# Performance work log

Measured on AMD Instinct MI355X. Metric: run time of the kernel, lower is better.

## Reference

```python
import jax, jax.numpy as jnp
import numpy as np

B, N, E, H, F, L, S = 4, 384, 768, 32, 3072, 12, 512
D = E // H


def setup_inputs() -> dict:
    key = jax.random.key(0)
    ks = jax.random.split(key, 32)
    inp = {}
    # forward args
    inp['node_type'] = jax.random.randint(ks[0], (B, N, 1), 1, S + 1)  # table has S+1 rows; 0 = pad (unused)
    inp['node_input_feature'] = jax.random.normal(ks[1], (B, N, E), jnp.float32)
    inp['in_degree'] = jax.random.randint(ks[2], (B, N), 0, S)
    inp['out_degree'] = jax.random.randint(ks[3], (B, N), 0, S)
    inp['attn_bias'] = jax.random.normal(ks[4], (B, N, N), jnp.float32) * 0.1
    inp['spatial_pos'] = jax.random.randint(ks[5], (B, N, N), 0, S)
    # embedding tables (normal stddev 0.02, as in the flax module)
    inp['node_emb'] = jax.random.normal(ks[6], (S + 1, E), jnp.float32) * 0.02
    inp['in_deg_emb'] = jax.random.normal(ks[7], (S, E), jnp.float32) * 0.02
    inp['out_deg_emb'] = jax.random.normal(ks[8], (S, E), jnp.float32) * 0.02
    inp['sp_emb'] = jax.random.normal(ks[9], (S, H), jnp.float32) * 0.02
    inp['sp_emb_rev'] = jax.random.normal(ks[10], (S, H), jnp.float32) * 0.02
    # per-layer weights, stacked along leading L axis
    se, sf = 1.0 / np.sqrt(E), 1.0 / np.sqrt(F)
    inp['Wq'] = jax.random.normal(ks[11], (L, E, E), jnp.float32) * se
    inp['bq'] = jax.random.normal(ks[12], (L, E), jnp.float32) * se
    inp['Wk'] = jax.random.normal(ks[13], (L, E, E), jnp.float32) * se
    inp['bk'] = jax.random.normal(ks[14], (L, E), jnp.float32) * se
    inp['Wv'] = jax.random.normal(ks[15], (L, E, E), jnp.float32) * se
    inp['bv'] = jax.random.normal(ks[16], (L, E), jnp.float32) * se
    inp['Wo'] = jax.random.normal(ks[17], (L, E, E), jnp.float32) * se
    inp['bo'] = jnp.zeros((L, E), jnp.float32)
    inp['W1'] = jax.random.normal(ks[18], (L, E, F), jnp.float32) * se
    inp['b1'] = jax.random.normal(ks[19], (L, F), jnp.float32) * se
    inp['W2'] = jax.random.normal(ks[20], (L, F, E), jnp.float32) * sf
    inp['b2'] = jax.random.normal(ks[21], (L, E), jnp.float32) * sf
    inp['ln1_s'] = jnp.ones((L, E), jnp.float32)
    inp['ln1_b'] = jnp.zeros((L, E), jnp.float32)
    inp['ln2_s'] = jnp.ones((L, E), jnp.float32)
    inp['ln2_b'] = jnp.zeros((L, E), jnp.float32)
    return inp


def _layernorm(x, scale, bias, eps=1e-5):
    m = x.mean(-1, keepdims=True)
    v = ((x - m) ** 2).mean(-1, keepdims=True)
    return (x - m) / jnp.sqrt(v + eps) * scale + bias


def _encoder(node_type, node_input_feature, in_degree, out_degree, attn_bias, spatial_pos,
             node_emb, in_deg_emb, out_deg_emb, sp_emb, sp_emb_rev,
             Wq, bq, Wk, bk, Wv, bv, Wo, bo, W1, b1, W2, b2, ln1_s, ln1_b, ln2_s, ln2_b):
    nt = node_type[..., 0]                               # [B,N]
    padding_mask = nt == 0                               # [B,N]
    # node features: node_emb(node_type).sum(-2) + degree embeddings + input feature
    x = (node_emb[node_type].sum(axis=-2)
         + in_deg_emb[in_degree] + out_deg_emb[out_degree]
         + node_input_feature)                           # [B,N,E]
    # spatial attention bias: [B,N,N,H] -> [B,H,N,N], plus graph-level attn_bias
    sb = sp_emb[spatial_pos] + sp_emb_rev[jnp.transpose(spatial_pos, (0, 2, 1))]
    bias = jnp.transpose(sb, (0, 3, 1, 2)) + attn_bias[:, None]  # [B,H,N,N]

    x = jnp.transpose(x, (1, 0, 2))                      # [N,B,E]
    scaling = D ** (-0.5)
    neg_inf = jnp.float32(-jnp.inf)

    def layer(x, p):
        wq, bq_, wk, bk_, wv, bv_, wo, bo_, w1, b1_, w2, b2_, s1, t1, s2, t2 = p
        q = ((x @ wq) + bq_) * scaling                   # [N,B,E], bias scaled too (faithful)
        k = (x @ wk) + bk_
        v = (x @ wv) + bv_
        q = q.reshape(N, B, H, D)
        k = k.reshape(N, B, H, D)
        v = v.reshape(N, B, H, D)
        w = jnp.einsum('nbhd,mbhd->bhnm', q, k) + bias   # [B,H,N,N]
        w = jnp.where(padding_mask[:, None, None, :], neg_inf, w)
        probs = jax.nn.softmax(w.astype(jnp.float32), axis=-1).astype(x.dtype)
        a = jnp.einsum('bhnm,mbhd->nbhd', probs, v).reshape(N, B, E)
        a = a @ wo + bo_
        x = _layernorm(x + a, s1, t1)                    # post-LN
        h = jax.nn.gelu(x @ w1 + b1_)                    # approximate gelu (flax default)
        h = h @ w2 + b2_
        x = _layernorm(x + h, s2, t2)
        return x, None

    xs = (Wq, bq, Wk, bk, Wv, bv, Wo, bo, W1, b1, W2, b2, ln1_s, ln1_b, ln2_s, ln2_b)
    x, _ = jax.lax.scan(layer, x, xs)
    return x                                             # [N,B,E]


def reference(node_type, node_input_feature, in_degree, out_degree, attn_bias, spatial_pos,
              node_emb, in_deg_emb, out_deg_emb, sp_emb, sp_emb_rev,
              Wq, bq, Wk, bk, Wv, bv, Wo, bo, W1, b1, W2, b2, ln1_s, ln1_b, ln2_s, ln2_b):
    return _encoder(node_type, node_input_feature, in_degree, out_degree, attn_bias, spatial_pos,
                    node_emb, in_deg_emb, out_deg_emb, sp_emb, sp_emb_rev,
                    Wq, bq, Wk, bk, Wv, bv, Wo, bo, W1, b1, W2, b2, ln1_s, ln1_b, ln2_s, ln2_b)
```

## Files before the change

kernel.cpp:

```cpp
#include <hip/hip_runtime.h>
#include <hip/hip_bf16.h>

#define Bb 4
#define Nn 384
#define Ee 768
#define Hh 32
#define Ff 3072
#define Ll 12
#define Ss 512
#define Mm (Nn*Bb)

typedef __attribute__((ext_vector_type(8))) short bf16x8;
typedef __attribute__((ext_vector_type(4))) float f32x4;
typedef unsigned short u16;

__device__ __forceinline__ u16 f2b(float f) {
  union { float f; unsigned int i; } c; c.f = f;
  unsigned int x = c.i;
  return (u16)((x + 0x7fffu + ((x >> 16) & 1u)) >> 16);
}
__device__ __forceinline__ float b2f(u16 u) {
  union { unsigned int i; float f; } c; c.i = ((unsigned int)u) << 16; return c.f;
}
__device__ __forceinline__ unsigned pkcvt(float lo, float hi) {
  unsigned r;
  asm("v_cvt_pk_bf16_f32 %0, %1, %2" : "=v"(r) : "v"(lo), "v"(hi));
  return r;
}
__device__ __forceinline__ void gload_lds16(const void* g, void* l) {
  __builtin_amdgcn_global_load_lds((__attribute__((address_space(1))) void*)(g),
                                   (__attribute__((address_space(3))) void*)(l), 16, 0, 0);
}

__global__ __launch_bounds__(256) void embed_kernel(
    const int* __restrict__ node_type, const float* __restrict__ nif,
    const int* __restrict__ in_deg, const int* __restrict__ out_deg,
    const float* __restrict__ node_emb, const float* __restrict__ ind_emb,
    const float* __restrict__ outd_emb,
    float* __restrict__ x, u16* __restrict__ xb)
{
  const int r = blockIdx.x;
  const int n = r / Bb, b = r % Bb;
  const int nt  = node_type[b*Nn + n];
  const int idg = in_deg[b*Nn + n];
  const int odg = out_deg[b*Nn + n];
  for (int c = threadIdx.x; c < Ee; c += 256) {
    float val = node_emb[(size_t)nt*Ee + c] + ind_emb[(size_t)idg*Ee + c]
              + outd_emb[(size_t)odg*Ee + c] + nif[((size_t)b*Nn + n)*Ee + c];
    x[(size_t)r*Ee + c] = val;
    xb[(size_t)r*Ee + c] = f2b(val);
  }
}

__global__ void spT_kernel(const int* __restrict__ sp, int* __restrict__ spT)
{
  __shared__ int tile[32][33];
  const int b = blockIdx.z;
  const int n0 = blockIdx.y * 32, m0 = blockIdx.x * 32;
  const int tx = threadIdx.x, ty = threadIdx.y;
  for (int i = ty; i < 32; i += 8)
    tile[i][tx] = sp[((size_t)b*Nn + n0 + i)*Nn + m0 + tx];
  __syncthreads();
  for (int i = ty; i < 32; i += 8)
    spT[((size_t)b*Nn + m0 + i)*Nn + n0 + tx] = tile[tx][i];
}

__global__ __launch_bounds__(256) void bias_pre_kernel(
    const float* __restrict__ atb, const int* __restrict__ sp, const int* __restrict__ spT,
    const float* __restrict__ sp_emb, const float* __restrict__ sp_emb_rev,
    u16* __restrict__ biasb)
{
  __shared__ float spc[512], sprc[512];
  const int bx = blockIdx.x, h = blockIdx.y, b = blockIdx.z;
  const int t = threadIdx.x;
  for (int i = t; i < 512; i += 256) {
    spc[i]  = sp_emb[(size_t)i*Hh + h];
    sprc[i] = sp_emb_rev[(size_t)i*Hh + h];
  }
  __syncthreads();
  const int q = bx*16 + ((t >> 2) & 15);
  const size_t rowb = ((size_t)b*Nn + q)*Nn;
  u16* outb = biasb + (((size_t)(b*Hh + h)*24 + bx)*24)*256 + t;
  const int mbase = ((t >> 6) << 2) + (t & 3);
  for (int tt = 0; tt < 24; ++tt) {
    const int m = tt*16 + mbase;
    float v = atb[rowb + m] + spc[sp[rowb + m]] + sprc[spT[rowb + m]];
    outb[tt*256] = f2b(v);
  }
}

__global__ __launch_bounds__(256) void wconv_kernel(
    const float* __restrict__ Wq, const float* __restrict__ Wk, const float* __restrict__ Wv,
    const float* __restrict__ Wo, const float* __restrict__ W1, const float* __restrict__ W2,
    int layer0, u16* __restrict__ wTall, unsigned slotStride)
{
  __shared__ float tile[64][65];
  const int layer = layer0 + blockIdx.y;
  u16* slot = wTall + (size_t)blockIdx.y * slotStride;
  int tid = blockIdx.x;
  const float* src; u16* dst; int Ns, Ks;
  if (tid < 432)       { int seg = tid / 144; tid -= seg*144;
                         src = (seg==0?Wq:(seg==1?Wk:Wv)) + (size_t)layer*Ee*Ee;
                         dst = slot + (size_t)seg*589824; Ns = 768; Ks = 768; }
  else if (tid < 576)  { tid -= 432; src = Wo + (size_t)layer*Ee*Ee; dst = slot + 1769472; Ns = 768;  Ks = 768; }
  else if (tid < 1152) { tid -= 576; src = W1 + (size_t)layer*Ee*Ff; dst = slot + 2359296; Ns = 3072; Ks = 768; }
  else                 { tid -= 1152; src = W2 + (size_t)layer*Ff*Ee; dst = slot + 4718592; Ns = 768; Ks = 3072; }
  const int tc = Ns >> 6;
  const int tk = tid / tc, tn = tid % tc;
  const int t = threadIdx.x;
  #pragma unroll
  for (int i = 0; i < 4; ++i) {
    const int id = t + i*256;
    const int r = id >> 4, c = (id & 15) << 2;
    float4 v = *(const float4*)(src + (size_t)(tk*64 + r)*Ns + tn*64 + c);
    tile[r][c+0] = v.x; tile[r][c+1] = v.y; tile[r][c+2] = v.z; tile[r][c+3] = v.w;
  }
  __syncthreads();
  #pragma unroll
  for (int i = 0; i < 2; ++i) {
    const int ch = t + i*256;
    const int n = ch >> 3, kc = (ch & 7) << 3;
    uint4 u;
    u.x = pkcvt(tile[kc+0][n], tile[kc+1][n]);
    u.y = pkcvt(tile[kc+2][n], tile[kc+3][n]);
    u.z = pkcvt(tile[kc+4][n], tile[kc+5][n]);
    u.w = pkcvt(tile[kc+6][n], tile[kc+7][n]);
    *(uint4*)(dst + (size_t)(tn*64 + n)*Ks + tk*64 + kc) = u;
  }
}

template<int EPI>
__global__ __launch_bounds__(256) void gemm3_kernel(
    const u16* __restrict__ A, const u16* __restrict__ Bw,
    const float* __restrict__ b0, const float* __restrict__ b1, const float* __restrict__ b2,
    int Kfull, int Kc, float scaleQ,
    float* __restrict__ outF, u16* __restrict__ outB)
{
  __shared__ __align__(16) u16 As[2][128][64];
  __shared__ __align__(16) u16 Bs[2][64][64];
  const int t = threadIdx.x, lane = t & 63, wave = t >> 6;
  int bx = blockIdx.x, by = blockIdx.y;
  {
    const int gx = gridDim.x;
    const int nwg = gx * gridDim.y;
    const int bid = bx + gx * by;
    const int cpx = nwg >> 3;
    const int s = (bid & 7) * cpx + (bid >> 3);
    bx = s % gx; by = s / gx;
  }
  const int m0 = bx * 128, n0 = by * 64;
  const int k0 = blockIdx.z * Kc;
  const int wm = wave >> 1, wn = wave & 1;
  const int ql = lane & 15, hi = lane >> 4;
  const int nk = Kc >> 6;
  const int sr = t >> 3;
  const int sslot = (t & 7) ^ (sr & 7);
  const size_t aoff = (size_t)(m0 + sr)*Kfull + k0 + (sslot << 3);
  const size_t boff = (size_t)(n0 + sr)*Kfull + k0 + (sslot << 3);
  const size_t rstep = (size_t)32 * Kfull;

  int aro[4][2], bro[2][2];
  #pragma unroll
  for (int ks = 0; ks < 2; ++ks) {
    const int kb = (((ks<<2) + hi) ^ (ql & 7)) << 4;
    #pragma unroll
    for (int f = 0; f < 4; ++f) aro[f][ks] = (wm*64 + f*16 + ql)*128 + kb;
    #pragma unroll
    for (int f = 0; f < 2; ++f) bro[f][ks] = (wn*32 + f*16 + ql)*128 + kb;
  }

  f32x4 acc[4][2];
  #pragma unroll
  for (int a = 0; a < 4; ++a)
    #pragma unroll
    for (int c = 0; c < 2; ++c) acc[a][c] = (f32x4){0.f,0.f,0.f,0.f};

  #pragma unroll
  for (int i = 0; i < 4; ++i)
    gload_lds16(A + aoff + i*rstep, (char*)&As[0][0][0] + i*4096 + t*16);
  #pragma unroll
  for (int i = 0; i < 2; ++i)
    gload_lds16(Bw + boff + i*rstep, (char*)&Bs[0][0][0] + i*4096 + t*16);

  for (int kt = 0; kt < nk; ++kt) {
    const int cur = kt & 1, nxt = cur ^ 1;
    const bool pre = (kt + 1 < nk);
    if (pre) {
      const size_t kk = (size_t)(kt + 1) << 6;
      #pragma unroll
      for (int i = 0; i < 4; ++i)
        gload_lds16(A + aoff + kk + i*rstep, (char*)&As[nxt][0][0] + i*4096 + t*16);
      #pragma unroll
      for (int i = 0; i < 2; ++i)
        gload_lds16(Bw + boff + kk + i*rstep, (char*)&Bs[nxt][0][0] + i*4096 + t*16);
      asm volatile("s_waitcnt vmcnt(6)" ::: "memory");
    } else {
      asm volatile("s_waitcnt vmcnt(0)" ::: "memory");
    }
    __builtin_amdgcn_s_barrier();
    __builtin_amdgcn_sched_barrier(0);

    const char* aBase = (const char*)&As[cur][0][0];
    const char* bBase = (const char*)&Bs[cur][0][0];
    bf16x8 af[4][2], bf[2][2];
    #pragma unroll
    for (int f = 0; f < 4; ++f)
      #pragma unroll
      for (int ks = 0; ks < 2; ++ks)
        af[f][ks] = *(const bf16x8*)(aBase + aro[f][ks]);
    #pragma unroll
    for (int f = 0; f < 2; ++f)
      #pragma unroll
      for (int ks = 0; ks < 2; ++ks)
        bf[f][ks] = *(const bf16x8*)(bBase + bro[f][ks]);
    #pragma unroll
    for (int ks = 0; ks < 2; ++ks)
      #pragma unroll
      for (int fm = 0; fm < 4; ++fm)
        #pragma unroll
        for (int fn = 0; fn < 2; ++fn)
          acc[fm][fn] = __builtin_amdgcn_mfma_f32_16x16x32_bf16(af[fm][ks], bf[fn][ks], acc[fm][fn], 0, 0, 0);
    if (pre) {
      __builtin_amdgcn_sched_barrier(0);
      __builtin_amdgcn_s_barrier();
    }
  }

  #pragma unroll
  for (int fm = 0; fm < 4; ++fm) {
    const int rowb = m0 + wm*64 + fm*16 + hi*4;
    #pragma unroll
    for (int fn = 0; fn < 2; ++fn) {
      const int gcol = n0 + wn*32 + fn*16 + ql;
      float bv, scale = 1.0f;
      if (EPI == 0) {
        const int seg = gcol / 768;
        const int cw = gcol - seg*768;
        bv = (seg == 0) ? b0[cw] : ((seg == 1) ? b1[cw] : b2[cw]);
        if (seg == 0) scale = scaleQ;
      } else if (EPI == 1) {
        bv = (blockIdx.z == 0) ? b0[gcol] : 0.0f;
      } else {
        bv = b0[gcol];
      }
      f32x4 v = acc[fm][fn];
      #pragma unroll
      for (int j = 0; j < 4; ++j) {
        float val = (v[j] + bv) * scale;
        if (EPI == 0) {
          outB[(size_t)(rowb + j) * 2304 + gcol] = f2b(val);
        } else if (EPI == 1) {
          outF[(size_t)blockIdx.z * (Mm*768) + (size_t)(rowb + j) * 768 + gcol] = val;
        } else {
          float arg = 0.7978845608028654f * (val + 0.044715f * val * val * val);
          float e = __expf(2.0f * arg);
          float g = 0.5f * val * (2.0f - 2.0f / (e + 1.0f));
          outB[(size_t)(rowb + j) * 3072 + gcol] = f2b(g);
        }
      }
    }
  }
}

template<int PREBIAS>
__global__ __launch_bounds__(256) void attn2_kernel(
    const u16* __restrict__ qkv,
    const u16* __restrict__ biasb,
    const float* __restrict__ atb, const int* __restrict__ sp, const int* __restrict__ spT,
    const float* __restrict__ sp_emb, const float* __restrict__ sp_emb_rev,
    u16* __restrict__ ab)
{
  __shared__ __align__(16) u16 Kt[384][32];
  __shared__ __align__(16) u16 Vt[32][392];
  __shared__ __align__(16) u16 Qt[64][32];
  __shared__ __align__(16) u16 Pw[4][16][32];
  __shared__ float spc[512], sprc[512];
  const int bid = blockIdx.x;
  const int pair = bid % 3;
  const int h = (bid / 3) % Hh;
  const int b = bid / (3 * Hh);
  const int t = threadIdx.x, lane = t & 63, wave = t >> 6;
  const int ql = lane & 15, hi = lane >> 4;

  for (int idx = t; idx < 384*6; idx += 256) {
    const int m = idx / 6, c = idx - m*6;
    const u16* base = qkv + ((size_t)m*Bb + b)*2304 + h*24 + c*4;
    uint2 kk = *(const uint2*)(base + 768);
    uint2 vv = *(const uint2*)(base + 1536);
    *(uint2*)&Kt[m][c*4] = kk;
    Vt[c*4+0][m] = (u16)(vv.x & 0xffffu); Vt[c*4+1][m] = (u16)(vv.x >> 16);
    Vt[c*4+2][m] = (u16)(vv.y & 0xffffu); Vt[c*4+3][m] = (u16)(vv.y >> 16);
  }
  for (int idx = t; idx < 384*2; idx += 256)
    *(uint2*)&Kt[idx>>1][24 + (idx&1)*4] = make_uint2(0u, 0u);
  for (int idx = t; idx < 8*196; idx += 256)
    *(unsigned*)((char*)&Vt[24][0] + idx*4) = 0u;
  if (!PREBIAS) {
    for (int i = t; i < 512; i += 256) {
      spc[i]  = sp_emb[(size_t)i*Hh + h];
      sprc[i] = sp_emb_rev[(size_t)i*Hh + h];
    }
  }

  for (int qi = 0; qi < 2; ++qi) {
    const int ntile = pair*2 + qi;
    for (int idx = t; idx < 64*6; idx += 256) {
      const int qr = idx / 6, c = idx - qr*6;
      const u16* base = qkv + ((size_t)(ntile*64 + qr)*Bb + b)*2304 + h*24 + c*4;
      *(uint2*)&Qt[qr][c*4] = *(const uint2*)base;
    }
    for (int idx = t; idx < 64*2; idx += 256)
      *(uint2*)&Qt[idx>>1][24 + (idx&1)*4] = make_uint2(0u, 0u);
    __syncthreads();

    const int q0 = ntile*64 + wave*16;
    const int q = q0 + ql;
    const bf16x8 qf = *(const bf16x8*)&Qt[wave*16 + ql][hi*8];

    f32x4 f[24];
    const u16* bp = biasb + (((size_t)(b*Hh + h)*24 + ntile*4 + wave)*24)*256 + lane*4;
    const size_t crow = ((size_t)b*Nn + q)*Nn;
    #pragma unroll
    for (int tt = 0; tt < 24; ++tt) {
      bf16x8 kf = *(const bf16x8*)&Kt[tt*16 + ql][hi*8];
      f32x4 z = (f32x4){0.f,0.f,0.f,0.f};
      f32x4 s = __builtin_amdgcn_mfma_f32_16x16x32_bf16(kf, qf, z, 0, 0, 0);
      if (PREBIAS) {
        uint2 bb = *(const uint2*)(bp + tt*256);
        s[0] += b2f((u16)(bb.x & 0xffffu)); s[1] += b2f((u16)(bb.x >> 16));
        s[2] += b2f((u16)(bb.y & 0xffffu)); s[3] += b2f((u16)(bb.y >> 16));
      } else {
        const int off = tt*16 + hi*4;
        int4 s4 = *(const int4*)(sp + crow + off);
        int4 t4 = *(const int4*)(spT + crow + off);
        float4 a4 = *(const float4*)(atb + crow + off);
        s[0] += a4.x + spc[s4.x] + sprc[t4.x];
        s[1] += a4.y + spc[s4.y] + sprc[t4.y];
        s[2] += a4.z + spc[s4.z] + sprc[t4.z];
        s[3] += a4.w + spc[s4.w] + sprc[t4.w];
      }
      f[tt] = s;
    }

    float mx = -3.0e38f;
    #pragma unroll
    for (int tt = 0; tt < 24; ++tt)
      mx = fmaxf(mx, fmaxf(fmaxf(f[tt][0], f[tt][1]), fmaxf(f[tt][2], f[tt][3])));
    mx = fmaxf(mx, __shfl_xor(mx, 16, 64));
    mx = fmaxf(mx, __shfl_xor(mx, 32, 64));
    float sum = 0.f;
    #pragma unroll
    for (int tt = 0; tt < 24; ++tt) {
      #pragma unroll
      for (int j = 0; j < 4; ++j) { f[tt][j] = __expf(f[tt][j] - mx); sum += f[tt][j]; }
    }
    sum += __shfl_xor(sum, 16, 64);
    sum += __shfl_xor(sum, 32, 64);
    const float inv = 1.0f / sum;

    f32x4 o0 = (f32x4){0.f,0.f,0.f,0.f}, o1 = (f32x4){0.f,0.f,0.f,0.f};
    char* prow = (char*)&Pw[wave][ql][0];
    const int swz = (ql & 3) << 4;
    #pragma unroll
    for (int c = 0; c < 12; ++c) {
      unsigned w0 = pkcvt(f[2*c][0],   f[2*c][1]);
      unsigned w1 = pkcvt(f[2*c][2],   f[2*c][3]);
      unsigned w2 = pkcvt(f[2*c+1][0], f[2*c+1][1]);
      unsigned w3 = pkcvt(f[2*c+1][2], f[2*c+1][3]);
      *(unsigned*)(prow + (((hi*8)      ) ^ swz)) = w0;
      *(unsigned*)(prow + (((hi*8) +  4) ^ swz)) = w1;
      *(unsigned*)(prow + (((hi*8) + 32) ^ swz)) = w2;
      *(unsigned*)(prow + (((hi*8) + 36) ^ swz)) = w3;
      bf16x8 a = *(const bf16x8*)(prow + ((hi*16) ^ swz));
      bf16x8 v0 = *(const bf16x8*)&Vt[ql][c*32 + hi*8];
      bf16x8 v1 = *(const bf16x8*)&Vt[16 + ql][c*32 + hi*8];
      o0 = __builtin_amdgcn_mfma_f32_16x16x32_bf16(a, v0, o0, 0, 0, 0);
      o1 = __builtin_amdgcn_mfma_f32_16x16x32_bf16(a, v1, o1, 0, 0, 0);
    }

    #pragma unroll
    for (int j = 0; j < 4; ++j) {
      float invj = __shfl(inv, hi*4 + j, 64);
      const int qg = q0 + hi*4 + j;
      u16* orow = ab + ((size_t)qg*Bb + b)*Ee + h*24;
      orow[ql] = f2b(o0[j] * invj);
      if (ql < 8) orow[16 + ql] = f2b(o1[j] * invj);
    }
    __syncthreads();
  }
}

template<int NP>
__global__ __launch_bounds__(256) void ln_kernel(
    const float* __restrict__ xin, const float* __restrict__ delta,
    const float* __restrict__ gamma, const float* __restrict__ beta,
    float* __restrict__ xout, u16* __restrict__ xb)
{
  __shared__ float red[8];
  const int r = blockIdx.x, t = threadIdx.x;
  const size_t base = (size_t)r * Ee;
  float v[3];
  #pragma unroll
  for (int i = 0; i < 3; ++i) {
    int c = t + i*256;
    float d = xin[base + c];
    #pragma unroll
    for (int p = 0; p < NP; ++p) d += delta[(size_t)p*(Mm*768) + base + c];
    v[i] = d;
  }
  float s = v[0] + v[1] + v[2];
  #pragma unroll
  for (int off = 1; off < 64; off <<= 1) s += __shfl_xor(s, off, 64);
  if ((t & 63) == 0) red[t >> 6] = s;
  __syncthreads();
  const float mean = (red[0] + red[1] + red[2] + red[3]) * (1.0f / 768.0f);
  float qs = 0.f;
  #pragma unroll
  for (int i = 0; i < 3; ++i) { float d = v[i] - mean; qs += d * d; }
  #pragma unroll
  for (int off = 1; off < 64; off <<= 1) qs += __shfl_xor(qs, off, 64);
  if ((t & 63) == 0) red[4 + (t >> 6)] = qs;
  __syncthreads();
  const float var = (red[4] + red[5] + red[6] + red[7]) * (1.0f / 768.0f);
  const float rstd = rsqrtf(var + 1e-5f);
  #pragma unroll
  for (int i = 0; i < 3; ++i) {
    int c = t + i*256;
    float o = (v[i] - mean) * rstd * gamma[c] + beta[c];
    xout[base + c] = o;
    xb[base + c] = f2b(o);
  }
}

extern "C" void kernel_launch(void* const* d_in, const int* in_sizes, int n_in,
                              void* d_out, int out_size, void* d_ws, size_t ws_size,
                              hipStream_t stream) {
  const int*   node_type  = (const int*)d_in[0];
  const float* nif        = (const float*)d_in[1];
  const int*   in_deg     = (const int*)d_in[2];
  const int*   out_deg    = (const int*)d_in[3];
  const float* atb        = (const float*)d_in[4];
  const int*   sp         = (const int*)d_in[5];
  const float* node_emb   = (const float*)d_in[6];
  const float* ind_emb    = (const float*)d_in[7];
  const float* outd_emb   = (const float*)d_in[8];
  const float* sp_emb     = (const float*)d_in[9];
  const float* sp_emb_rev = (const float*)d_in[10];
  const float* Wq = (const float*)d_in[11]; const float* bq = (const float*)d_in[12];
  const float* Wk = (const float*)d_in[13]; const float* bk = (const float*)d_in[14];
  const float* Wv = (const float*)d_in[15]; const float* bv = (const float*)d_in[16];
  const float* Wo = (const float*)d_in[17]; const float* bo = (const float*)d_in[18];
  const float* W1 = (const float*)d_in[19]; const float* b1 = (const float*)d_in[20];
  const float* W2 = (const float*)d_in[21]; const float* b2 = (const float*)d_in[22];
  const float* ln1s = (const float*)d_in[23]; const float* ln1b = (const float*)d_in[24];
  const float* ln2s = (const float*)d_in[25]; const float* ln2b = (const float*)d_in[26];

  char* ws = (char*)d_ws;
  float* x      = (float*)(ws);
  u16*   xb     = (u16*)(ws +  4718592);
  u16*   qkvb16 = (u16*)(ws +  7077888);
  u16*   abuf   = (u16*)(ws + 14155776);
  u16*   hb     = (u16*)(ws + 16515072);
  float* obufP  = (float*)(ws + 25952256);
  int*   spTb   = (int*)(ws + 44826624);
  u16*   biasb  = (u16*)(ws + 47185920);
  const bool useBias = ws_size >= 99090432ull;
  const bool allW    = ws_size >= 254803968ull;
  u16* wTall = (u16*)(ws + (useBias ? 84934656 : 47185920));
  const unsigned LSLOT = 7077888u;

  embed_kernel<<<Mm, 256, 0, stream>>>(node_type, nif, in_deg, out_deg,
                                       node_emb, ind_emb, outd_emb, x, xb);
  spT_kernel<<<dim3(12, 12, 4), dim3(32, 8), 0, stream>>>(sp, spTb);
  if (useBias)
    bias_pre_kernel<<<dim3(24, 32, 4), 256, 0, stream>>>(atb, sp, spTb, sp_emb, sp_emb_rev, biasb);
  if (allW)
    wconv_kernel<<<dim3(1728, 12), 256, 0, stream>>>(Wq, Wk, Wv, Wo, W1, W2,
                                                     0, wTall, LSLOT);

  const float scaleQ = 0.2041241452319315f;

  for (int l = 0; l < Ll; ++l) {
    const float *bql = bq + (size_t)l*Ee, *bkl = bk + (size_t)l*Ee, *bvl = bv + (size_t)l*Ee;
    const float *bol = bo + (size_t)l*Ee;
    const float *b1l = b1 + (size_t)l*Ff, *b2l = b2 + (size_t)l*Ee;

    if (!allW)
      wconv_kernel<<<dim3(1728, 1), 256, 0, stream>>>(Wq, Wk, Wv, Wo, W1, W2,
                                                      l, wTall, 0u);
    u16* slot = wTall + (size_t)(allW ? l : 0) * LSLOT;
    const u16* qkvT = slot;
    const u16* woT  = slot + 1769472;
    const u16* w1T  = slot + 2359296;
    const u16* w2T  = slot + 4718592;

    gemm3_kernel<0><<<dim3(12, 36), 256, 0, stream>>>(xb, qkvT, bql, bkl, bvl,
                                                      768, 768, scaleQ, nullptr, qkvb16);
    if (useBias)
      attn2_kernel<1><<<384, 256, 0, stream>>>(qkvb16, biasb, atb, sp, spTb,
                                               sp_emb, sp_emb_rev, abuf);
    else
      attn2_kernel<0><<<384, 256, 0, stream>>>(qkvb16, nullptr, atb, sp, spTb,
                                               sp_emb, sp_emb_rev, abuf);
    gemm3_kernel<1><<<dim3(12, 12, 2), 256, 0, stream>>>(abuf, woT, bol, bol, bol,
                                                         768, 384, 1.0f, obufP, nullptr);
    ln_kernel<2><<<Mm, 256, 0, stream>>>(x, obufP, ln1s + (size_t)l*Ee, ln1b + (size_t)l*Ee, x, xb);
    gemm3_kernel<2><<<dim3(12, 48), 256, 0, stream>>>(xb, w1T, b1l, b1l, b1l,
                                                      768, 768, 1.0f, nullptr, hb);
    gemm3_kernel<1><<<dim3(12, 12, 4), 256, 0, stream>>>(hb, w2T, b2l, b2l, b2l,
                                                         3072, 768, 1.0f, obufP, nullptr);
    float* xdst = (l == Ll - 1) ? (float*)d_out : x;
    ln_kernel<4><<<Mm, 256, 0, stream>>>(x, obufP, ln2s + (size_t)l*Ee, ln2b + (size_t)l*Ee, xdst, xb);
  }
}
```

Baseline: 1.347 ms.

## Widen GEMM tile to 128x128 with 512 threads, batch weight conversion tiles

```diff
diff --git a/kernel.cpp b/kernel.cpp
--- a/kernel.cpp
+++ b/kernel.cpp
@@ -89,6 +89,22 @@
   }
 }
 
+__device__ __forceinline__ void wc_resolve(int tid, int layer,
+    const float* Wq, const float* Wk, const float* Wv, const float* Wo,
+    const float* W1, const float* W2, u16* slot,
+    const float*& src, u16*& dst, int& Ns, int& Ks, int& tk, int& tn)
+{
+  if (tid < 432)      { int seg = tid/144; int r = tid - seg*144;
+                        src = (seg==0?Wq:(seg==1?Wk:Wv)) + (size_t)layer*Ee*Ee;
+                        dst = slot + (size_t)seg*589824; Ns=768; Ks=768; tk=r/12; tn=r%12; }
+  else if (tid < 576) { int r = tid-432;  src = Wo + (size_t)layer*Ee*Ee;
+                        dst = slot + 1769472; Ns=768;  Ks=768;  tk=r/12; tn=r%12; }
+  else if (tid < 1152){ int r = tid-576;  src = W1 + (size_t)layer*Ee*Ff;
+                        dst = slot + 2359296; Ns=3072; Ks=768;  tk=r/48; tn=r%48; }
+  else                { int r = tid-1152; src = W2 + (size_t)layer*Ff*Ee;
+                        dst = slot + 4718592; Ns=768;  Ks=3072; tk=r/12; tn=r%12; }
+}
+
 __global__ __launch_bounds__(256) void wconv_kernel(
     const float* __restrict__ Wq, const float* __restrict__ Wk, const float* __restrict__ Wv,
     const float* __restrict__ Wo, const float* __restrict__ W1, const float* __restrict__ W2,
@@ -97,47 +113,56 @@
   __shared__ float tile[64][65];
   const int layer = layer0 + blockIdx.y;
   u16* slot = wTall + (size_t)blockIdx.y * slotStride;
-  int tid = blockIdx.x;
-  const float* src; u16* dst; int Ns, Ks;
-  if (tid < 432)       { int seg = tid / 144; tid -= seg*144;
-                         src = (seg==0?Wq:(seg==1?Wk:Wv)) + (size_t)layer*Ee*Ee;
-                         dst = slot + (size_t)seg*589824; Ns = 768; Ks = 768; }
-  else if (tid < 576)  { tid -= 432; src = Wo + (size_t)layer*Ee*Ee; dst = slot + 1769472; Ns = 768;  Ks = 768; }
-  else if (tid < 1152) { tid -= 576; src = W1 + (size_t)layer*Ee*Ff; dst = slot + 2359296; Ns = 3072; Ks = 768; }
-  else                 { tid -= 1152; src = W2 + (size_t)layer*Ff*Ee; dst = slot + 4718592; Ns = 768; Ks = 3072; }
-  const int tc = Ns >> 6;
-  const int tk = tid / tc, tn = tid % tc;
   const int t = threadIdx.x;
-  #pragma unroll
-  for (int i = 0; i < 4; ++i) {
-    const int id = t + i*256;
-    const int r = id >> 4, c = (id & 15) << 2;
-    float4 v = *(const float4*)(src + (size_t)(tk*64 + r)*Ns + tn*64 + c);
-    tile[r][c+0] = v.x; tile[r][c+1] = v.y; tile[r][c+2] = v.z; tile[r][c+3] = v.w;
-  }
-  __syncthreads();
-  #pragma unroll
-  for (int i = 0; i < 2; ++i) {
-    const int ch = t + i*256;
-    const int n = ch >> 3, kc = (ch & 7) << 3;
-    uint4 u;
-    u.x = pkcvt(tile[kc+0][n], tile[kc+1][n]);
-    u.y = pkcvt(tile[kc+2][n], tile[kc+3][n]);
-    u.z = pkcvt(tile[kc+4][n], tile[kc+5][n]);
-    u.w = pkcvt(tile[kc+6][n], tile[kc+7][n]);
-    *(uint4*)(dst + (size_t)(tn*64 + n)*Ks + tk*64 + kc) = u;
+  const int lr = t >> 4, c0 = (t & 15) << 2;
+  const int tid0 = blockIdx.x * 6;
+
+  const float* src; u16* dst; int Ns, Ks, tk, tn;
+  wc_resolve(tid0, layer, Wq, Wk, Wv, Wo, W1, W2, slot, src, dst, Ns, Ks, tk, tn);
+  float4 rg[4];
+  #pragma unroll
+  for (int i = 0; i < 4; ++i)
+    rg[i] = *(const float4*)(src + (size_t)(tk*64 + lr + i*16)*Ns + tn*64 + c0);
+
+  for (int it = 0; it < 6; ++it) {
+    u16* dstC = dst; const int KsC = Ks, tkC = tk, tnC = tn;
+    __syncthreads();
+    #pragma unroll
+    for (int i = 0; i < 4; ++i) {
+      float4 v = rg[i];
+      const int r = lr + i*16;
+      tile[r][c0+0] = v.x; tile[r][c0+1] = v.y; tile[r][c0+2] = v.z; tile[r][c0+3] = v.w;
+    }
+    if (it + 1 < 6) {
+      wc_resolve(tid0 + it + 1, layer, Wq, Wk, Wv, Wo, W1, W2, slot, src, dst, Ns, Ks, tk, tn);
+      #pragma unroll
+      for (int i = 0; i < 4; ++i)
+        rg[i] = *(const float4*)(src + (size_t)(tk*64 + lr + i*16)*Ns + tn*64 + c0);
+    }
+    __syncthreads();
+    #pragma unroll
+    for (int i = 0; i < 2; ++i) {
+      const int ch = t + i*256;
+      const int n = ch >> 3, kc = (ch & 7) << 3;
+      uint4 u;
+      u.x = pkcvt(tile[kc+0][n], tile[kc+1][n]);
+      u.y = pkcvt(tile[kc+2][n], tile[kc+3][n]);
+      u.z = pkcvt(tile[kc+4][n], tile[kc+5][n]);
+      u.w = pkcvt(tile[kc+6][n], tile[kc+7][n]);
+      *(uint4*)(dstC + (size_t)(tnC*64 + n)*KsC + tkC*64 + kc) = u;
+    }
   }
 }
 
 template<int EPI>
-__global__ __launch_bounds__(256) void gemm3_kernel(
+__global__ __launch_bounds__(512) void gemm4_kernel(
     const u16* __restrict__ A, const u16* __restrict__ Bw,
     const float* __restrict__ b0, const float* __restrict__ b1, const float* __restrict__ b2,
     int Kfull, int Kc, float scaleQ,
     float* __restrict__ outF, u16* __restrict__ outB)
 {
   __shared__ __align__(16) u16 As[2][128][64];
-  __shared__ __align__(16) u16 Bs[2][64][64];
+  __shared__ __align__(16) u16 Bs[2][128][64];
   const int t = threadIdx.x, lane = t & 63, wave = t >> 6;
   int bx = blockIdx.x, by = blockIdx.y;
   {
@@ -148,16 +173,16 @@
     const int s = (bid & 7) * cpx + (bid >> 3);
     bx = s % gx; by = s / gx;
   }
-  const int m0 = bx * 128, n0 = by * 64;
+  const int m0 = bx * 128, n0 = by * 128;
   const int k0 = blockIdx.z * Kc;
-  const int wm = wave >> 1, wn = wave & 1;
+  const int wm = wave >> 2, wn = wave & 3;
   const int ql = lane & 15, hi = lane >> 4;
   const int nk = Kc >> 6;
   const int sr = t >> 3;
   const int sslot = (t & 7) ^ (sr & 7);
   const size_t aoff = (size_t)(m0 + sr)*Kfull + k0 + (sslot << 3);
   const size_t boff = (size_t)(n0 + sr)*Kfull + k0 + (sslot << 3);
-  const size_t rstep = (size_t)32 * Kfull;
+  const size_t rstep = (size_t)64 * Kfull;
 
   int aro[4][2], bro[2][2];
   #pragma unroll
@@ -176,11 +201,10 @@
     for (int c = 0; c < 2; ++c) acc[a][c] = (f32x4){0.f,0.f,0.f,0.f};
 
   #pragma unroll
-  for (int i = 0; i < 4; ++i)
-    gload_lds16(A + aoff + i*rstep, (char*)&As[0][0][0] + i*4096 + t*16);
-  #pragma unroll
-  for (int i = 0; i < 2; ++i)
-    gload_lds16(Bw + boff + i*rstep, (char*)&Bs[0][0][0] + i*4096 + t*16);
+  for (int i = 0; i < 2; ++i) {
+    gload_lds16(A  + aoff + i*rstep, (char*)&As[0][0][0] + i*8192 + t*16);
+    gload_lds16(Bw + boff + i*rstep, (char*)&Bs[0][0][0] + i*8192 + t*16);
+  }
 
   for (int kt = 0; kt < nk; ++kt) {
     const int cur = kt & 1, nxt = cur ^ 1;
@@ -188,12 +212,11 @@
     if (pre) {
       const size_t kk = (size_t)(kt + 1) << 6;
       #pragma unroll
-      for (int i = 0; i < 4; ++i)
-        gload_lds16(A + aoff + kk + i*rstep, (char*)&As[nxt][0][0] + i*4096 + t*16);
-      #pragma unroll
-      for (int i = 0; i < 2; ++i)
-        gload_lds16(Bw + boff + kk + i*rstep, (char*)&Bs[nxt][0][0] + i*4096 + t*16);
-      asm volatile("s_waitcnt vmcnt(6)" ::: "memory");
+      for (int i = 0; i < 2; ++i) {
+        gload_lds16(A  + aoff + kk + i*rstep, (char*)&As[nxt][0][0] + i*8192 + t*16);
+        gload_lds16(Bw + boff + kk + i*rstep, (char*)&Bs[nxt][0][0] + i*8192 + t*16);
+      }
+      asm volatile("s_waitcnt vmcnt(4)" ::: "memory");
     } else {
       asm volatile("s_waitcnt vmcnt(0)" ::: "memory");
     }
@@ -295,6 +318,8 @@
     *(uint2*)&Kt[idx>>1][24 + (idx&1)*4] = make_uint2(0u, 0u);
   for (int idx = t; idx < 8*196; idx += 256)
     *(unsigned*)((char*)&Vt[24][0] + idx*4) = 0u;
+  for (int idx = t; idx < 64*2; idx += 256)
+    *(uint2*)&Qt[idx>>1][24 + (idx&1)*4] = make_uint2(0u, 0u);
   if (!PREBIAS) {
     for (int i = t; i < 512; i += 256) {
       spc[i]  = sp_emb[(size_t)i*Hh + h];
@@ -309,8 +334,6 @@
       const u16* base = qkv + ((size_t)(ntile*64 + qr)*Bb + b)*2304 + h*24 + c*4;
       *(uint2*)&Qt[qr][c*4] = *(const uint2*)base;
     }
-    for (int idx = t; idx < 64*2; idx += 256)
-      *(uint2*)&Qt[idx>>1][24 + (idx&1)*4] = make_uint2(0u, 0u);
     __syncthreads();
 
     const int q0 = ntile*64 + wave*16;
@@ -475,8 +498,8 @@
   if (useBias)
     bias_pre_kernel<<<dim3(24, 32, 4), 256, 0, stream>>>(atb, sp, spTb, sp_emb, sp_emb_rev, biasb);
   if (allW)
-    wconv_kernel<<<dim3(1728, 12), 256, 0, stream>>>(Wq, Wk, Wv, Wo, W1, W2,
-                                                     0, wTall, LSLOT);
+    wconv_kernel<<<dim3(288, 12), 256, 0, stream>>>(Wq, Wk, Wv, Wo, W1, W2,
+                                                    0, wTall, LSLOT);
 
   const float scaleQ = 0.2041241452319315f;
 
@@ -486,15 +509,15 @@
     const float *b1l = b1 + (size_t)l*Ff, *b2l = b2 + (size_t)l*Ee;
 
     if (!allW)
-      wconv_kernel<<<dim3(1728, 1), 256, 0, stream>>>(Wq, Wk, Wv, Wo, W1, W2,
-                                                      l, wTall, 0u);
+      wconv_kernel<<<dim3(288, 1), 256, 0, stream>>>(Wq, Wk, Wv, Wo, W1, W2,
+                                                     l, wTall, 0u);
     u16* slot = wTall + (size_t)(allW ? l : 0) * LSLOT;
     const u16* qkvT = slot;
     const u16* woT  = slot + 1769472;
     const u16* w1T  = slot + 2359296;
     const u16* w2T  = slot + 4718592;
 
-    gemm3_kernel<0><<<dim3(12, 36), 256, 0, stream>>>(xb, qkvT, bql, bkl, bvl,
+    gemm4_kernel<0><<<dim3(12, 18), 512, 0, stream>>>(xb, qkvT, bql, bkl, bvl,
                                                       768, 768, scaleQ, nullptr, qkvb16);
     if (useBias)
       attn2_kernel<1><<<384, 256, 0, stream>>>(qkvb16, biasb, atb, sp, spTb,
@@ -502,13 +525,13 @@
     else
       attn2_kernel<0><<<384, 256, 0, stream>>>(qkvb16, nullptr, atb, sp, spTb,
                                                sp_emb, sp_emb_rev, abuf);
-    gemm3_kernel<1><<<dim3(12, 12, 2), 256, 0, stream>>>(abuf, woT, bol, bol, bol,
-                                                         768, 384, 1.0f, obufP, nullptr);
-    ln_kernel<2><<<Mm, 256, 0, stream>>>(x, obufP, ln1s + (size_t)l*Ee, ln1b + (size_t)l*Ee, x, xb);
-    gemm3_kernel<2><<<dim3(12, 48), 256, 0, stream>>>(xb, w1T, b1l, b1l, b1l,
+    gemm4_kernel<1><<<dim3(12, 6, 4), 512, 0, stream>>>(abuf, woT, bol, bol, bol,
+                                                        768, 192, 1.0f, obufP, nullptr);
+    ln_kernel<4><<<Mm, 256, 0, stream>>>(x, obufP, ln1s + (size_t)l*Ee, ln1b + (size_t)l*Ee, x, xb);
+    gemm4_kernel<2><<<dim3(12, 24), 512, 0, stream>>>(xb, w1T, b1l, b1l, b1l,
                                                       768, 768, 1.0f, nullptr, hb);
-    gemm3_kernel<1><<<dim3(12, 12, 4), 256, 0, stream>>>(hb, w2T, b2l, b2l, b2l,
-                                                         3072, 768, 1.0f, obufP, nullptr);
+    gemm4_kernel<1><<<dim3(12, 6, 4), 512, 0, stream>>>(hb, w2T, b2l, b2l, b2l,
+                                                        3072, 768, 1.0f, obufP, nullptr);
     float* xdst = (l == Ll - 1) ? (float*)d_out : x;
     ln_kernel<4><<<Mm, 256, 0, stream>>>(x, obufP, ln2s + (size_t)l*Ee, ln2b + (size_t)l*Ee, xdst, xb);
   }
```

After: 1.434 ms. 6.5% more time.

## Store weights in k-blocked bf16 layout, fold residual into GEMM epilogue, halve W2 split-K

Applied to the files above, without the earlier changes.

```diff
diff --git a/kernel.cpp b/kernel.cpp
--- a/kernel.cpp
+++ b/kernel.cpp
@@ -89,43 +89,62 @@
   }
 }
 
+__device__ __forceinline__ void wc3_resolve(int tid, int layer,
+    const float* Wq, const float* Wk, const float* Wv, const float* Wo,
+    const float* W1, const float* W2, u16* slot,
+    const float*& src, u16*& dst, int& Ns, int& kb, int& nc)
+{
+  if (tid < 1152)      { int seg = tid/288; int r = tid - seg*288;
+                         src = (seg==0?Wq:(seg==1?Wk:(seg==2?Wv:Wo))) + (size_t)layer*Ee*Ee;
+                         dst = slot + (size_t)(seg<3 ? seg*589824 : 1769472);
+                         Ns = 768; kb = r/3; nc = r%3; }
+  else if (tid < 2304) { int r = tid-1152; src = W1 + (size_t)layer*Ee*Ff;
+                         dst = slot + 2359296; Ns = 3072; kb = r/12; nc = r%12; }
+  else                 { int r = tid-2304; src = W2 + (size_t)layer*Ff*Ee;
+                         dst = slot + 4718592; Ns = 768;  kb = r/3;  nc = r%3; }
+}
+
 __global__ __launch_bounds__(256) void wconv_kernel(
     const float* __restrict__ Wq, const float* __restrict__ Wk, const float* __restrict__ Wv,
     const float* __restrict__ Wo, const float* __restrict__ W1, const float* __restrict__ W2,
     int layer0, u16* __restrict__ wTall, unsigned slotStride)
 {
-  __shared__ float tile[64][65];
+  __shared__ __align__(16) float buf[2][2048];
+  const int t = threadIdx.x;
   const int layer = layer0 + blockIdx.y;
   u16* slot = wTall + (size_t)blockIdx.y * slotStride;
-  int tid = blockIdx.x;
-  const float* src; u16* dst; int Ns, Ks;
-  if (tid < 432)       { int seg = tid / 144; tid -= seg*144;
-                         src = (seg==0?Wq:(seg==1?Wk:Wv)) + (size_t)layer*Ee*Ee;
-                         dst = slot + (size_t)seg*589824; Ns = 768; Ks = 768; }
-  else if (tid < 576)  { tid -= 432; src = Wo + (size_t)layer*Ee*Ee; dst = slot + 1769472; Ns = 768;  Ks = 768; }
-  else if (tid < 1152) { tid -= 576; src = W1 + (size_t)layer*Ee*Ff; dst = slot + 2359296; Ns = 3072; Ks = 768; }
-  else                 { tid -= 1152; src = W2 + (size_t)layer*Ff*Ee; dst = slot + 4718592; Ns = 768; Ks = 3072; }
-  const int tc = Ns >> 6;
-  const int tk = tid / tc, tn = tid % tc;
-  const int t = threadIdx.x;
-  #pragma unroll
-  for (int i = 0; i < 4; ++i) {
-    const int id = t + i*256;
-    const int r = id >> 4, c = (id & 15) << 2;
-    float4 v = *(const float4*)(src + (size_t)(tk*64 + r)*Ns + tn*64 + c);
-    tile[r][c+0] = v.x; tile[r][c+1] = v.y; tile[r][c+2] = v.z; tile[r][c+3] = v.w;
-  }
-  __syncthreads();
-  #pragma unroll
-  for (int i = 0; i < 2; ++i) {
-    const int ch = t + i*256;
-    const int n = ch >> 3, kc = (ch & 7) << 3;
+  const int tid0 = blockIdx.x * 8;
+  const int lrow = t >> 6, lcol = (t & 63) << 2;
+
+  const float* src; u16* dst; int Ns, kb, nc;
+  wc3_resolve(tid0, layer, Wq, Wk, Wv, Wo, W1, W2, slot, src, dst, Ns, kb, nc);
+  #pragma unroll
+  for (int i = 0; i < 2; ++i)
+    gload_lds16(src + (size_t)(kb*8 + i*4 + lrow)*Ns + nc*256 + lcol,
+                (char*)&buf[0][0] + i*4096 + t*16);
+
+  for (int it = 0; it < 8; ++it) {
+    const int cur = it & 1;
+    u16* dstC = dst; const int NsC = Ns, kbC = kb, ncC = nc;
+    if (it + 1 < 8) {
+      wc3_resolve(tid0 + it + 1, layer, Wq, Wk, Wv, Wo, W1, W2, slot, src, dst, Ns, kb, nc);
+      #pragma unroll
+      for (int i = 0; i < 2; ++i)
+        gload_lds16(src + (size_t)(kb*8 + i*4 + lrow)*Ns + nc*256 + lcol,
+                    (char*)&buf[cur^1][0] + i*4096 + t*16);
+      asm volatile("s_waitcnt vmcnt(2)" ::: "memory");
+    } else {
+      asm volatile("s_waitcnt vmcnt(0)" ::: "memory");
+    }
+    __builtin_amdgcn_s_barrier();
+    const float* bc = &buf[cur][0];
     uint4 u;
-    u.x = pkcvt(tile[kc+0][n], tile[kc+1][n]);
-    u.y = pkcvt(tile[kc+2][n], tile[kc+3][n]);
-    u.z = pkcvt(tile[kc+4][n], tile[kc+5][n]);
-    u.w = pkcvt(tile[kc+6][n], tile[kc+7][n]);
-    *(uint4*)(dst + (size_t)(tn*64 + n)*Ks + tk*64 + kc) = u;
+    u.x = pkcvt(bc[0*256 + t], bc[1*256 + t]);
+    u.y = pkcvt(bc[2*256 + t], bc[3*256 + t]);
+    u.z = pkcvt(bc[4*256 + t], bc[5*256 + t]);
+    u.w = pkcvt(bc[6*256 + t], bc[7*256 + t]);
+    *(uint4*)(dstC + (size_t)kbC*NsC*8 + (size_t)(ncC*256 + t)*8) = u;
+    __builtin_amdgcn_s_barrier();
   }
 }
 
@@ -133,11 +152,12 @@
 __global__ __launch_bounds__(256) void gemm3_kernel(
     const u16* __restrict__ A, const u16* __restrict__ Bw,
     const float* __restrict__ b0, const float* __restrict__ b1, const float* __restrict__ b2,
-    int Kfull, int Kc, float scaleQ,
+    const float* __restrict__ resid,
+    int Kfull, int Ns8, int Kc, float scaleQ,
     float* __restrict__ outF, u16* __restrict__ outB)
 {
   __shared__ __align__(16) u16 As[2][128][64];
-  __shared__ __align__(16) u16 Bs[2][64][64];
+  __shared__ __align__(16) u16 Bs[2][4096];
   const int t = threadIdx.x, lane = t & 63, wave = t >> 6;
   int bx = blockIdx.x, by = blockIdx.y;
   {
@@ -153,20 +173,29 @@
   const int wm = wave >> 1, wn = wave & 1;
   const int ql = lane & 15, hi = lane >> 4;
   const int nk = Kc >> 6;
+  int n0loc = n0; size_t bsegoff = 0;
+  if (EPI == 0) { const int seg = n0 / 768; n0loc = n0 - seg*768; bsegoff = (size_t)seg*589824; }
   const int sr = t >> 3;
   const int sslot = (t & 7) ^ (sr & 7);
   const size_t aoff = (size_t)(m0 + sr)*Kfull + k0 + (sslot << 3);
-  const size_t boff = (size_t)(n0 + sr)*Kfull + k0 + (sslot << 3);
   const size_t rstep = (size_t)32 * Kfull;
+  const int c0kb = t >> 6,        c0j = t & 63;
+  const int c1kb = (t + 256) >> 6, c1j = t & 63;
+  const size_t bo0 = bsegoff + (size_t)c0kb*Ns8 + (size_t)(n0loc + (c0j ^ (c0kb & 7)))*8;
+  const size_t bo1 = bsegoff + (size_t)c1kb*Ns8 + (size_t)(n0loc + (c1j ^ (c1kb & 7)))*8;
+  const int kb0base = k0 >> 3;
 
   int aro[4][2], bro[2][2];
   #pragma unroll
   for (int ks = 0; ks < 2; ++ks) {
-    const int kb = (((ks<<2) + hi) ^ (ql & 7)) << 4;
-    #pragma unroll
-    for (int f = 0; f < 4; ++f) aro[f][ks] = (wm*64 + f*16 + ql)*128 + kb;
-    #pragma unroll
-    for (int f = 0; f < 2; ++f) bro[f][ks] = (wn*32 + f*16 + ql)*128 + kb;
+    const int kbA = (((ks<<2) + hi) ^ (ql & 7)) << 4;
+    #pragma unroll
+    for (int f = 0; f < 4; ++f) aro[f][ks] = (wm*64 + f*16 + ql)*128 + kbA;
+    #pragma unroll
+    for (int f = 0; f < 2; ++f) {
+      const int kbB = (ks<<2) + hi;
+      bro[f][ks] = ((kbB*64) + ((wn*32 + f*16 + ql) ^ kbB)) << 4;
+    }
   }
 
   f32x4 acc[4][2];
@@ -178,9 +207,8 @@
   #pragma unroll
   for (int i = 0; i < 4; ++i)
     gload_lds16(A + aoff + i*rstep, (char*)&As[0][0][0] + i*4096 + t*16);
-  #pragma unroll
-  for (int i = 0; i < 2; ++i)
-    gload_lds16(Bw + boff + i*rstep, (char*)&Bs[0][0][0] + i*4096 + t*16);
+  gload_lds16(Bw + (size_t)kb0base*Ns8 + bo0, (char*)&Bs[0][0] + t*16);
+  gload_lds16(Bw + (size_t)kb0base*Ns8 + bo1, (char*)&Bs[0][0] + 4096 + t*16);
 
   for (int kt = 0; kt < nk; ++kt) {
     const int cur = kt & 1, nxt = cur ^ 1;
@@ -190,9 +218,9 @@
       #pragma unroll
       for (int i = 0; i < 4; ++i)
         gload_lds16(A + aoff + kk + i*rstep, (char*)&As[nxt][0][0] + i*4096 + t*16);
-      #pragma unroll
-      for (int i = 0; i < 2; ++i)
-        gload_lds16(Bw + boff + kk + i*rstep, (char*)&Bs[nxt][0][0] + i*4096 + t*16);
+      const size_t kbrow = (size_t)(kb0base + (kt + 1)*8)*Ns8;
+      gload_lds16(Bw + kbrow + bo0, (char*)&Bs[nxt][0] + t*16);
+      gload_lds16(Bw + kbrow + bo1, (char*)&Bs[nxt][0] + 4096 + t*16);
       asm volatile("s_waitcnt vmcnt(6)" ::: "memory");
     } else {
       asm volatile("s_waitcnt vmcnt(0)" ::: "memory");
@@ -201,7 +229,7 @@
     __builtin_amdgcn_sched_barrier(0);
 
     const char* aBase = (const char*)&As[cur][0][0];
-    const char* bBase = (const char*)&Bs[cur][0][0];
+    const char* bBase = (const char*)&Bs[cur][0];
     bf16x8 af[4][2], bf[2][2];
     #pragma unroll
     for (int f = 0; f < 4; ++f)
@@ -232,7 +260,7 @@
     #pragma unroll
     for (int fn = 0; fn < 2; ++fn) {
       const int gcol = n0 + wn*32 + fn*16 + ql;
-      float bv, scale = 1.0f;
+      float bv = 0.f, scale = 1.0f;
       if (EPI == 0) {
         const int seg = gcol / 768;
         const int cw = gcol - seg*768;
@@ -250,6 +278,7 @@
         if (EPI == 0) {
           outB[(size_t)(rowb + j) * 2304 + gcol] = f2b(val);
         } else if (EPI == 1) {
+          if (blockIdx.z == 0) val += resid[(size_t)(rowb + j) * 768 + gcol];
           outF[(size_t)blockIdx.z * (Mm*768) + (size_t)(rowb + j) * 768 + gcol] = val;
         } else {
           float arg = 0.7978845608028654f * (val + 0.044715f * val * val * val);
@@ -295,6 +324,8 @@
     *(uint2*)&Kt[idx>>1][24 + (idx&1)*4] = make_uint2(0u, 0u);
   for (int idx = t; idx < 8*196; idx += 256)
     *(unsigned*)((char*)&Vt[24][0] + idx*4) = 0u;
+  for (int idx = t; idx < 64*2; idx += 256)
+    *(uint2*)&Qt[idx>>1][24 + (idx&1)*4] = make_uint2(0u, 0u);
   if (!PREBIAS) {
     for (int i = t; i < 512; i += 256) {
       spc[i]  = sp_emb[(size_t)i*Hh + h];
@@ -309,8 +340,6 @@
       const u16* base = qkv + ((size_t)(ntile*64 + qr)*Bb + b)*2304 + h*24 + c*4;
       *(uint2*)&Qt[qr][c*4] = *(const uint2*)base;
     }
-    for (int idx = t; idx < 64*2; idx += 256)
-      *(uint2*)&Qt[idx>>1][24 + (idx&1)*4] = make_uint2(0u, 0u);
     __syncthreads();
 
     const int q0 = ntile*64 + wave*16;
@@ -392,7 +421,7 @@
 
 template<int NP>
 __global__ __launch_bounds__(256) void ln_kernel(
-    const float* __restrict__ xin, const float* __restrict__ delta,
+    const float* __restrict__ delta,
     const float* __restrict__ gamma, const float* __restrict__ beta,
     float* __restrict__ xout, u16* __restrict__ xb)
 {
@@ -403,7 +432,7 @@
   #pragma unroll
   for (int i = 0; i < 3; ++i) {
     int c = t + i*256;
-    float d = xin[base + c];
+    float d = 0.f;
     #pragma unroll
     for (int p = 0; p < NP; ++p) d += delta[(size_t)p*(Mm*768) + base + c];
     v[i] = d;
@@ -475,8 +504,8 @@
   if (useBias)
     bias_pre_kernel<<<dim3(24, 32, 4), 256, 0, stream>>>(atb, sp, spTb, sp_emb, sp_emb_rev, biasb);
   if (allW)
-    wconv_kernel<<<dim3(1728, 12), 256, 0, stream>>>(Wq, Wk, Wv, Wo, W1, W2,
-                                                     0, wTall, LSLOT);
+    wconv_kernel<<<dim3(432, 12), 256, 0, stream>>>(Wq, Wk, Wv, Wo, W1, W2,
+                                                    0, wTall, LSLOT);
 
   const float scaleQ = 0.2041241452319315f;
 
@@ -486,30 +515,30 @@
     const float *b1l = b1 + (size_t)l*Ff, *b2l = b2 + (size_t)l*Ee;
 
     if (!allW)
-      wconv_kernel<<<dim3(1728, 1), 256, 0, stream>>>(Wq, Wk, Wv, Wo, W1, W2,
-                                                      l, wTall, 0u);
+      wconv_kernel<<<dim3(432, 1), 256, 0, stream>>>(Wq, Wk, Wv, Wo, W1, W2,
+                                                     l, wTall, 0u);
     u16* slot = wTall + (size_t)(allW ? l : 0) * LSLOT;
     const u16* qkvT = slot;
     const u16* woT  = slot + 1769472;
     const u16* w1T  = slot + 2359296;
     const u16* w2T  = slot + 4718592;
 
-    gemm3_kernel<0><<<dim3(12, 36), 256, 0, stream>>>(xb, qkvT, bql, bkl, bvl,
-                                                      768, 768, scaleQ, nullptr, qkvb16);
+    gemm3_kernel<0><<<dim3(12, 36), 256, 0, stream>>>(xb, qkvT, bql, bkl, bvl, x,
+                                                      768, 6144, 768, scaleQ, nullptr, qkvb16);
     if (useBias)
       attn2_kernel<1><<<384, 256, 0, stream>>>(qkvb16, biasb, atb, sp, spTb,
                                                sp_emb, sp_emb_rev, abuf);
     else
       attn2_kernel<0><<<384, 256, 0, stream>>>(qkvb16, nullptr, atb, sp, spTb,
                                                sp_emb, sp_emb_rev, abuf);
-    gemm3_kernel<1><<<dim3(12, 12, 2), 256, 0, stream>>>(abuf, woT, bol, bol, bol,
-                                                         768, 384, 1.0f, obufP, nullptr);
-    ln_kernel<2><<<Mm, 256, 0, stream>>>(x, obufP, ln1s + (size_t)l*Ee, ln1b + (size_t)l*Ee, x, xb);
-    gemm3_kernel<2><<<dim3(12, 48), 256, 0, stream>>>(xb, w1T, b1l, b1l, b1l,
-                                                      768, 768, 1.0f, nullptr, hb);
-    gemm3_kernel<1><<<dim3(12, 12, 4), 256, 0, stream>>>(hb, w2T, b2l, b2l, b2l,
-                                                         3072, 768, 1.0f, obufP, nullptr);
+    gemm3_kernel<1><<<dim3(12, 12, 2), 256, 0, stream>>>(abuf, woT, bol, bol, bol, x,
+                                                         768, 6144, 384, 1.0f, obufP, nullptr);
+    ln_kernel<2><<<Mm, 256, 0, stream>>>(obufP, ln1s + (size_t)l*Ee, ln1b + (size_t)l*Ee, x, xb);
+    gemm3_kernel<2><<<dim3(12, 48), 256, 0, stream>>>(xb, w1T, b1l, b1l, b1l, x,
+                                                      768, 24576, 768, 1.0f, nullptr, hb);
+    gemm3_kernel<1><<<dim3(12, 12, 2), 256, 0, stream>>>(hb, w2T, b2l, b2l, b2l, x,
+                                                         3072, 6144, 1536, 1.0f, obufP, nullptr);
     float* xdst = (l == Ll - 1) ? (float*)d_out : x;
-    ln_kernel<4><<<Mm, 256, 0, stream>>>(x, obufP, ln2s + (size_t)l*Ee, ln2b + (size_t)l*Ee, xdst, xb);
-  }
-}
+    ln_kernel<2><<<Mm, 256, 0, stream>>>(obufP, ln2s + (size_t)l*Ee, ln2b + (size_t)l*Ee, xdst, xb);
+  }
+}
```

Result: slower. 1.591 ms (+18.2%).
